# Optimization experiments

Hardware: AMD Instinct MI355X
Metric: run time of the kernel (lower is better)

## Reference

```python
import jax, jax.numpy as jnp
import numpy as np

N = 100_000      # nodes
E = 3_200_000    # edges (avg degree 32)
F_IN = 100       # raw feature dim (embedding Linear(100, 64))
H = 64           # in/hidden/out channels
C = 18           # class_num
EPS = 1e-12      # F.normalize eps


def _sage_conv(x, src, dst, edge_weight, Wl, bl, Wr):
    """PyG-style SAGEConv: mean-aggregate neighbor messages, two linears, L2 normalize."""
    msg = x[src]                                   # [E, d] gather of x_j
    if edge_weight is not None:
        msg = msg * edge_weight[:, None]
    agg = jax.ops.segment_sum(msg, dst, num_segments=N)                       # [N, d]
    deg = jax.ops.segment_sum(jnp.ones((src.shape[0],), x.dtype), dst, num_segments=N)
    mean = agg / jnp.maximum(deg, 1.0)[:, None]
    out = mean @ Wl + bl + x @ Wr                  # lin_l(aggr) + lin_r(root)
    nrm = jnp.sqrt(jnp.sum(out * out, axis=-1, keepdims=True))
    return out / jnp.maximum(nrm, EPS)


def setup_inputs() -> dict:
    key = jax.random.key(0)
    ks = jax.random.split(key, 16)
    s = 0.1
    inp = {
        "x": jax.random.normal(ks[0], (N, F_IN), jnp.float32),
        "edge_index": jax.random.randint(ks[1], (2, E), 0, N, dtype=jnp.int64),
        "edge_weight": jax.random.uniform(ks[2], (E,), jnp.float32),
        "emb_W": jax.random.normal(ks[3], (F_IN, H), jnp.float32) * s,
        "emb_b": jnp.zeros((H,), jnp.float32),
    }
    k = 4
    for i in (1, 2, 3):
        inp[f"Wl{i}"] = jax.random.normal(ks[k], (H, H), jnp.float32) * s; k += 1
        inp[f"bl{i}"] = jnp.zeros((H,), jnp.float32)
        inp[f"Wr{i}"] = jax.random.normal(ks[k], (H, H), jnp.float32) * s; k += 1
    inp["Wl4"] = jax.random.normal(ks[k], (H, C), jnp.float32) * s; k += 1
    inp["bl4"] = jnp.zeros((C,), jnp.float32)
    inp["Wr4"] = jax.random.normal(ks[k], (H, C), jnp.float32) * s
    return inp


def reference(x, edge_index, edge_weight, emb_W, emb_b,
              Wl1, bl1, Wr1, Wl2, bl2, Wr2, Wl3, bl3, Wr3,
              Wl4, bl4, Wr4):
    src, dst = edge_index[0], edge_index[1]
    h = jax.nn.relu(x @ emb_W + emb_b)             # embedding MLP
    for Wl, bl, Wr in ((Wl1, bl1, Wr1), (Wl2, bl2, Wr2), (Wl3, bl3, Wr3)):
        h = jax.nn.relu(_sage_conv(h, src, dst, edge_weight, Wl, bl, Wr))
        # dropout p=0.2 is identity in eval mode
    return _sage_conv(h, src, dst, None, Wl4, bl4, Wr4)
```

## Files before the change

kernel.cpp:

```cpp
#include <hip/hip_runtime.h>
#include <hip/hip_bf16.h>

#define N_NODES   100000
#define N_EDGES   3200000
#define F_IN      100
#define H_DIM     64
#define C_NUM     18
#define NPB       1024
#define N_BKT     98
#define EPB       8192

typedef __attribute__((ext_vector_type(8))) short short8;
typedef __attribute__((ext_vector_type(4))) float f32x4;

__device__ __forceinline__ float ldf(const void* p, long long i, int isbf) {
    if (isbf) return __bfloat162float(((const __hip_bfloat16*)p)[i]);
    return ((const float*)p)[i];
}
__device__ __forceinline__ int ldi(const void* p, long long i, int is64) {
    if (is64) return (int)(((const long long*)p)[i]);
    return ((const int*)p)[i];
}
__device__ __forceinline__ unsigned short f2us(float f) {
    __hip_bfloat16 b = __float2bfloat16(f);
    return *(unsigned short*)&b;
}

__global__ void detect_kernel(const void* ei, const void* x, int* flags)
{
    if (threadIdx.x != 0 || blockIdx.x != 0) return;
    const long long* e64 = (const long long*)ei;
    int ok64 = 1;
    for (int i = 0; i < 128; ++i) {
        long long v = e64[i];
        if (v < 0 || v >= N_NODES) { ok64 = 0; break; }
    }
    const __hip_bfloat16* xb = (const __hip_bfloat16*)x;
    int cnt = 0;
    for (int i = 0; i < 256; ++i) {
        float v = fabsf(__bfloat162float(xb[i]));
        if (v == 0.0f || (v > 9.5367431640625e-7f && v < 1.0e6f)) ++cnt;
    }
    flags[0] = ok64;
    flags[1] = (cnt >= 240) ? 1 : 0;
}

__global__ void zero98(int* __restrict__ pcnt)
{
    int i = threadIdx.x;
    if (i < N_BKT) pcnt[i] = 0;
}

__global__ __launch_bounds__(1024) void radix_count(const void* ei, int* __restrict__ pcnt,
                                                    const int* __restrict__ flags)
{
    __shared__ int hist[N_BKT];
    const int t = threadIdx.x;
    if (t < N_BKT) hist[t] = 0;
    __syncthreads();
    const int base = blockIdx.x * EPB;
    const int n = min(EPB, N_EDGES - base);
    const int is64 = flags[0];
    for (int j = t; j < n; j += 1024) {
        int d = ldi(ei, (long long)N_EDGES + base + j, is64);
        atomicAdd(&hist[d >> 10], 1);
    }
    __syncthreads();
    if (t < N_BKT) atomicAdd(&pcnt[t], hist[t]);
}

__global__ void scan98(const int* __restrict__ cnt, int* __restrict__ base,
                       int* __restrict__ cursor)
{
    __shared__ int tmp[128];
    const int t = threadIdx.x;
    int v = (t < N_BKT) ? cnt[t] : 0;
    tmp[t] = v;
    __syncthreads();
    for (int off = 1; off < 128; off <<= 1) {
        int add = (t >= off) ? tmp[t - off] : 0;
        __syncthreads();
        tmp[t] += add;
        __syncthreads();
    }
    if (t < N_BKT) { base[t] = tmp[t] - v; cursor[t] = tmp[t] - v; }
    if (t == 127) base[N_BKT] = tmp[127];
}

__global__ __launch_bounds__(1024) void radix_scatter(const void* ei, const void* ew,
                                                      int* __restrict__ gcursor,
                                                      uint2* __restrict__ temp,
                                                      const int* __restrict__ flags)
{
    __shared__ uint2 stage[EPB];
    __shared__ unsigned char stgb[EPB];
    __shared__ int hist[128], scan_s[128];
    __shared__ int gbase[N_BKT], lcur[N_BKT];
    const int t = threadIdx.x;
    if (t < 128) hist[t] = 0;
    __syncthreads();

    const int base = blockIdx.x * EPB;
    const int n = min(EPB, N_EDGES - base);
    const int is64 = flags[0], isbf = flags[1];

    int  bkt[8];
    uint2 pk[8];
#pragma unroll
    for (int j = 0; j < 8; ++j) {
        int i = j * 1024 + t;
        bkt[j] = -1;
        if (i < n) {
            int e = base + i;
            int s = ldi(ei, e, is64);
            int d = ldi(ei, (long long)N_EDGES + e, is64);
            float w = ldf(ew, e, isbf);
            bkt[j] = d >> 10;
            pk[j].x = (unsigned)s | ((unsigned)(d & (NPB - 1)) << 17);
            pk[j].y = (unsigned)f2us(w);
            atomicAdd(&hist[bkt[j]], 1);
        }
    }
    __syncthreads();
    if (t < 128) scan_s[t] = hist[t];
    __syncthreads();
    for (int off = 1; off < 128; off <<= 1) {
        int add = 0;
        if (t < 128 && t >= off) add = scan_s[t - off];
        __syncthreads();
        if (t < 128) scan_s[t] += add;
        __syncthreads();
    }
    if (t < N_BKT) {
        int excl = scan_s[t] - hist[t];
        lcur[t] = excl;
        gbase[t] = atomicAdd(&gcursor[t], hist[t]) - excl;
    }
    __syncthreads();
#pragma unroll
    for (int j = 0; j < 8; ++j) {
        if (bkt[j] >= 0) {
            int pos = atomicAdd(&lcur[bkt[j]], 1);
            stage[pos] = pk[j];
            stgb[pos] = (unsigned char)bkt[j];
        }
    }
    __syncthreads();
#pragma unroll
    for (int j = 0; j < 8; ++j) {
        int i = j * 1024 + t;
        if (i < n) {
            int b = stgb[i];
            temp[gbase[b] + i] = stage[i];
        }
    }
}

__global__ __launch_bounds__(1024) void csr_build(const uint2* __restrict__ temp,
                          const int* __restrict__ pbase,
                          unsigned int* __restrict__ csr_pk,
                          int* __restrict__ deg, int* __restrict__ row_start,
                          float* __restrict__ inv_deg)
{
    __shared__ int cnt[NPB], scan_s[NPB], cur[NPB];
    const int b = blockIdx.x;
    const int t = threadIdx.x;
    cnt[t] = 0;
    __syncthreads();
    const int bs = pbase[b];
    const int be = pbase[b + 1];
    for (int i = bs + t; i < be; i += NPB)
        atomicAdd(&cnt[(temp[i].x >> 17) & (NPB - 1)], 1);
    __syncthreads();
    int v = cnt[t];
    scan_s[t] = v;
    __syncthreads();
    for (int off = 1; off < NPB; off <<= 1) {
        int add = (t >= off) ? scan_s[t - off] : 0;
        __syncthreads();
        scan_s[t] += add;
        __syncthreads();
    }
    int excl = bs + scan_s[t] - v;
    cur[t] = excl;
    int node = b * NPB + t;
    if (node < N_NODES) {
        deg[node]       = v;
        row_start[node] = excl;
        inv_deg[node]   = 1.0f / (float)max(v, 1);
    }
    __syncthreads();
    for (int i = bs + t; i < be; i += NPB) {
        uint2 e = temp[i];
        int k = (e.x >> 17) & (NPB - 1);
        int pos = atomicAdd(&cur[k], 1);
        csr_pk[pos] = (e.x & 0x1FFFFu) | ((e.y & 0x7FFFu) << 17);
    }
}

__global__ void embed_mfma(const void* x, const void* W, const void* b,
                           __hip_bfloat16* __restrict__ h, const int* __restrict__ flags)
{
    constexpr int KP = 136;
    __shared__ unsigned short W_s[H_DIM * KP];
    __shared__ float b_s[H_DIM];
    const int t = threadIdx.x;
    const int isbf = flags[1];
    for (int i = t; i < 128 * H_DIM; i += 256) {
        int k = i >> 6, n = i & 63;
        float v = (k < F_IN) ? ldf(W, (long long)k * H_DIM + n, isbf) : 0.0f;
        W_s[n * KP + k] = f2us(v);
    }
    if (t < H_DIM) b_s[t] = ldf(b, t, isbf);
    __syncthreads();

    const int wave = t >> 6, lane = t & 63, c = lane & 15, quad = lane >> 4;
    short8 bfrag[4][4];
#pragma unroll
    for (int nt = 0; nt < 4; ++nt)
#pragma unroll
        for (int kt = 0; kt < 4; ++kt)
            bfrag[nt][kt] = *(const short8*)&W_s[(nt * 16 + c) * KP + kt * 32 + quad * 8];

    const int nb = (blockIdx.x * 4 + wave) * 16;
    if (nb >= N_NODES) return;
    int node = nb + c; if (node >= N_NODES) node = N_NODES - 1;

    short8 afrag[4];
#pragma unroll
    for (int kt = 0; kt < 4; ++kt) {
        short8 a;
#pragma unroll
        for (int j = 0; j < 8; ++j) {
            int k = kt * 32 + quad * 8 + j;
            float v = (k < F_IN) ? ldf(x, (long long)node * F_IN + k, isbf) : 0.0f;
            a[j] = (short)f2us(v);
        }
        afrag[kt] = a;
    }

    f32x4 acc[4] = {};
#pragma unroll
    for (int nt = 0; nt < 4; ++nt)
#pragma unroll
        for (int kt = 0; kt < 4; ++kt)
            acc[nt] = __builtin_amdgcn_mfma_f32_16x16x32_bf16(afrag[kt], bfrag[nt][kt], acc[nt], 0, 0, 0);

#pragma unroll
    for (int nt = 0; nt < 4; ++nt)
#pragma unroll
        for (int reg = 0; reg < 4; ++reg) {
            int nn = nb + quad * 4 + reg;
            int col = nt * 16 + c;
            if (nn < N_NODES) {
                float v = fmaxf(acc[nt][reg] + b_s[col], 0.0f);
                h[(size_t)nn * H_DIM + col] = __float2bfloat16(v);
            }
        }
}

template <bool USE_W>
__global__ void gather_mean(const __hip_bfloat16* __restrict__ h,
                            const unsigned int* __restrict__ csr_pk,
                            const int* __restrict__ row_start,
                            const int* __restrict__ deg,
                            const float* __restrict__ inv_deg,
                            __hip_bfloat16* __restrict__ mean)
{
    const int lane = threadIdx.x & 63;
    const int c = lane & 7;
    const int r = lane >> 3;
    const int wid = blockIdx.x * 4 + (threadIdx.x >> 6);
    const int nw  = gridDim.x * 4;

    for (int n = wid; n < N_NODES; n += nw) {
        const int start = row_start[n];
        const int d     = deg[n];
        unsigned int ev = 0;
        if (lane < d) ev = csr_pk[start + lane];
        const int dmain = min(d, 64);
        float a0 = 0.f, a1 = 0.f, a2 = 0.f, a3 = 0.f;
        float a4 = 0.f, a5 = 0.f, a6 = 0.f, a7 = 0.f;
#pragma unroll 2
        for (int j0 = 0; j0 < dmain; j0 += 8) {
            unsigned int e = __shfl(ev, j0 + r);
            int s = e & 0x1FFFF;
            float w;
            if (USE_W) w = __uint_as_float((e & 0xFFFE0000u) >> 1);
            else       w = (j0 + r < dmain) ? 1.0f : 0.0f;
            uint4 hv = *(const uint4*)(h + (size_t)s * H_DIM + 8 * c);
            a0 = fmaf(w, __uint_as_float(hv.x << 16),          a0);
            a1 = fmaf(w, __uint_as_float(hv.x & 0xFFFF0000u),  a1);
            a2 = fmaf(w, __uint_as_float(hv.y << 16),          a2);
            a3 = fmaf(w, __uint_as_float(hv.y & 0xFFFF0000u),  a3);
            a4 = fmaf(w, __uint_as_float(hv.z << 16),          a4);
            a5 = fmaf(w, __uint_as_float(hv.z & 0xFFFF0000u),  a5);
            a6 = fmaf(w, __uint_as_float(hv.w << 16),          a6);
            a7 = fmaf(w, __uint_as_float(hv.w & 0xFFFF0000u),  a7);
        }
        for (int j = 64 + r; j < d; j += 8) {
            unsigned int e = csr_pk[start + j];
            int s = e & 0x1FFFF;
            float w = USE_W ? __uint_as_float((e & 0xFFFE0000u) >> 1) : 1.0f;
            uint4 hv = *(const uint4*)(h + (size_t)s * H_DIM + 8 * c);
            a0 = fmaf(w, __uint_as_float(hv.x << 16),          a0);
            a1 = fmaf(w, __uint_as_float(hv.x & 0xFFFF0000u),  a1);
            a2 = fmaf(w, __uint_as_float(hv.y << 16),          a2);
            a3 = fmaf(w, __uint_as_float(hv.y & 0xFFFF0000u),  a3);
            a4 = fmaf(w, __uint_as_float(hv.z << 16),          a4);
            a5 = fmaf(w, __uint_as_float(hv.z & 0xFFFF0000u),  a5);
            a6 = fmaf(w, __uint_as_float(hv.w << 16),          a6);
            a7 = fmaf(w, __uint_as_float(hv.w & 0xFFFF0000u),  a7);
        }
#pragma unroll
        for (int m = 8; m <= 32; m <<= 1) {
            a0 += __shfl_xor(a0, m); a1 += __shfl_xor(a1, m);
            a2 += __shfl_xor(a2, m); a3 += __shfl_xor(a3, m);
            a4 += __shfl_xor(a4, m); a5 += __shfl_xor(a5, m);
            a6 += __shfl_xor(a6, m); a7 += __shfl_xor(a7, m);
        }
        if (r == 0) {
            float inv = inv_deg[n];
            uint4 st;
            st.x = (unsigned)f2us(a0 * inv) | ((unsigned)f2us(a1 * inv) << 16);
            st.y = (unsigned)f2us(a2 * inv) | ((unsigned)f2us(a3 * inv) << 16);
            st.z = (unsigned)f2us(a4 * inv) | ((unsigned)f2us(a5 * inv) << 16);
            st.w = (unsigned)f2us(a6 * inv) | ((unsigned)f2us(a7 * inv) << 16);
            *(uint4*)(mean + (size_t)n * H_DIM + 8 * c) = st;
        }
    }
}

template <int COUT, bool RELU, bool FINAL>
__global__ void transform_mfma(const __hip_bfloat16* __restrict__ meanp,
                               const __hip_bfloat16* __restrict__ hp,
                               const void* Wl, const void* bl, const void* Wr,
                               __hip_bfloat16* __restrict__ h_out,
                               const int* __restrict__ flags, void* dout)
{
    constexpr int CP = (COUT + 15) & ~15;
    constexpr int NT = CP / 16;
    constexpr int KP = 136;
    __shared__ unsigned short W_s[CP * KP];
    __shared__ float b_s[CP];
    const int t = threadIdx.x;
    const int isbf = flags[1];
    for (int i = t; i < 128 * CP; i += 256) {
        int k = i / CP, n = i % CP;
        float v = 0.0f;
        if (n < COUT)
            v = (k < 64) ? ldf(Wl, (long long)k * COUT + n, isbf)
                         : ldf(Wr, (long long)(k - 64) * COUT + n, isbf);
        W_s[n * KP + k] = f2us(v);
    }
    if (t < CP) b_s[t] = (t < COUT) ? ldf(bl, t, isbf) : 0.0f;
    __syncthreads();

    const int wave = t >> 6, lane = t & 63, c = lane & 15, quad = lane >> 4;
    short8 bfrag[NT][4];
#pragma unroll
    for (int nt = 0; nt < NT; ++nt)
#pragma unroll
        for (int kt = 0; kt < 4; ++kt)
            bfrag[nt][kt] = *(const short8*)&W_s[(nt * 16 + c) * KP + kt * 32 + quad * 8];

    const int nb = (blockIdx.x * 4 + wave) * 16;
    if (nb >= N_NODES) return;
    int node = nb + c; if (node >= N_NODES) node = N_NODES - 1;

    short8 afrag[4];
#pragma unroll
    for (int kt = 0; kt < 4; ++kt) {
        const __hip_bfloat16* sp = (kt < 2) ? meanp : hp;
        afrag[kt] = *(const short8*)(sp + (size_t)node * H_DIM + (kt & 1) * 32 + quad * 8);
    }

    f32x4 acc[NT] = {};
#pragma unroll
    for (int nt = 0; nt < NT; ++nt)
#pragma unroll
        for (int kt = 0; kt < 4; ++kt)
            acc[nt] = __builtin_amdgcn_mfma_f32_16x16x32_bf16(afrag[kt], bfrag[nt][kt], acc[nt], 0, 0, 0);

    float rs[4];
#pragma unroll
    for (int reg = 0; reg < 4; ++reg) {
        float s2 = 0.f;
#pragma unroll
        for (int nt = 0; nt < NT; ++nt) {
            float v = acc[nt][reg] + b_s[nt * 16 + c];
            acc[nt][reg] = v;
            s2 += v * v;
        }
        s2 += __shfl_xor(s2, 1); s2 += __shfl_xor(s2, 2);
        s2 += __shfl_xor(s2, 4); s2 += __shfl_xor(s2, 8);
        rs[reg] = 1.0f / fmaxf(sqrtf(s2), 1e-12f);
    }

#pragma unroll
    for (int nt = 0; nt < NT; ++nt)
#pragma unroll
        for (int reg = 0; reg < 4; ++reg) {
            int nn  = nb + quad * 4 + reg;
            int col = nt * 16 + c;
            if (nn < N_NODES && col < COUT) {
                float v = acc[nt][reg] * rs[reg];
                if (RELU) v = fmaxf(v, 0.0f);
                if (FINAL) {
                    if (isbf) ((__hip_bfloat16*)dout)[(size_t)nn * COUT + col] = __float2bfloat16(v);
                    else      ((float*)dout)[(size_t)nn * COUT + col] = v;
                } else {
                    h_out[(size_t)nn * H_DIM + col] = __float2bfloat16(v);
                }
            }
        }
}

extern "C" void kernel_launch(void* const* d_in, const int* in_sizes, int n_in,
                              void* d_out, int out_size, void* d_ws, size_t ws_size,
                              hipStream_t stream)
{
    const void* x    = d_in[0];
    const void* ei   = d_in[1];
    const void* ew   = d_in[2];
    const void* embW = d_in[3];
    const void* embB = d_in[4];
    const void* Wl1 = d_in[5];  const void* bl1 = d_in[6];  const void* Wr1 = d_in[7];
    const void* Wl2 = d_in[8];  const void* bl2 = d_in[9];  const void* Wr2 = d_in[10];
    const void* Wl3 = d_in[11]; const void* bl3 = d_in[12]; const void* Wr3 = d_in[13];
    const void* Wl4 = d_in[14]; const void* bl4 = d_in[15]; const void* Wr4 = d_in[16];
    (void)in_sizes; (void)n_in; (void)out_size; (void)ws_size;

    char* ws = (char*)d_ws;
    size_t off = 0;
    auto alloc = [&](size_t bytes) -> void* {
        void* p = ws + off;
        off += (bytes + 255) & ~(size_t)255;
        return p;
    };
    uint2* temp = (uint2*)alloc((size_t)N_EDGES * sizeof(uint2));
    __hip_bfloat16* hA = (__hip_bfloat16*)temp;
    __hip_bfloat16* hB = (__hip_bfloat16*)((char*)temp + (size_t)N_NODES * H_DIM * 2);
    unsigned int* csr_pk = (unsigned int*)alloc((size_t)N_EDGES * sizeof(unsigned int));
    int*   pcnt    = (int*)  alloc((N_BKT)     * sizeof(int));
    int*   pbase   = (int*)  alloc((N_BKT + 1) * sizeof(int));
    int*   pcursor = (int*)  alloc((N_BKT)     * sizeof(int));
    int*   deg     = (int*)  alloc((size_t)N_NODES * sizeof(int));
    int*   row_st  = (int*)  alloc((size_t)N_NODES * sizeof(int));
    float* inv_deg = (float*)alloc((size_t)N_NODES * sizeof(float));
    int*   flags   = (int*)  alloc(256);

    const int NBr = (N_EDGES + EPB - 1) / EPB;
    const int NBt = (N_NODES + 63) / 64;

    detect_kernel<<<1, 64, 0, stream>>>(ei, x, flags);
    zero98<<<1, 128, 0, stream>>>(pcnt);
    radix_count<<<NBr, 1024, 0, stream>>>(ei, pcnt, flags);
    scan98<<<1, 128, 0, stream>>>(pcnt, pbase, pcursor);
    radix_scatter<<<NBr, 1024, 0, stream>>>(ei, ew, pcursor, temp, flags);
    csr_build<<<N_BKT, NPB, 0, stream>>>(temp, pbase, csr_pk, deg, row_st, inv_deg);

    embed_mfma<<<NBt, 256, 0, stream>>>(x, embW, embB, hA, flags);

    gather_mean<true><<<2048, 256, 0, stream>>>(hA, csr_pk, row_st, deg, inv_deg, hB);
    transform_mfma<H_DIM, true, false><<<NBt, 256, 0, stream>>>(
        hB, hA, Wl1, bl1, Wr1, hB, flags, d_out);
    gather_mean<true><<<2048, 256, 0, stream>>>(hB, csr_pk, row_st, deg, inv_deg, hA);
    transform_mfma<H_DIM, true, false><<<NBt, 256, 0, stream>>>(
        hA, hB, Wl2, bl2, Wr2, hA, flags, d_out);
    gather_mean<true><<<2048, 256, 0, stream>>>(hA, csr_pk, row_st, deg, inv_deg, hB);
    transform_mfma<H_DIM, true, false><<<NBt, 256, 0, stream>>>(
        hB, hA, Wl3, bl3, Wr3, hB, flags, d_out);
    gather_mean<false><<<2048, 256, 0, stream>>>(hB, csr_pk, row_st, deg, inv_deg, hA);
    transform_mfma<C_NUM, false, true><<<NBt, 256, 0, stream>>>(
        hA, hB, Wl4, bl4, Wr4, nullptr, flags, d_out);
}
```

Measured before the change: 551.4 us.

## Fuse neighbor mean aggregation with SAGE transform via shared-memory mean tile

Merges the gather_mean and transform_mfma kernels into one sage_fused kernel. Each block aggregates 64 nodes into a shared-memory mean tile, then runs the MFMA transform and normalization directly from it, which removes the global round trip of the mean tensor and four kernel launches. The embedding kernel now stages the x tile in shared memory with coalesced loads, and weight staging writes vectorized short8 rows. The gather now uses a fixed grid of 1563 blocks with 16 nodes per wave done sequentially, replacing the 2048-block grid-stride loop. This may reduce latency hiding and occupancy for the irregular gather, and the larger shared-memory footprint per block adds further occupancy pressure.

```diff
diff --git a/kernel.cpp b/kernel.cpp
--- a/kernel.cpp
+++ b/kernel.cpp
@@ -203,15 +203,50 @@
 {
     constexpr int KP = 136;
     __shared__ unsigned short W_s[H_DIM * KP];
+    __shared__ unsigned short x_s[64 * KP];
     __shared__ float b_s[H_DIM];
     const int t = threadIdx.x;
     const int isbf = flags[1];
-    for (int i = t; i < 128 * H_DIM; i += 256) {
-        int k = i >> 6, n = i & 63;
-        float v = (k < F_IN) ? ldf(W, (long long)k * H_DIM + n, isbf) : 0.0f;
-        W_s[n * KP + k] = f2us(v);
+
+    {
+        const int n0 = t >> 4, k8 = t & 15;
+        for (int n = n0; n < H_DIM; n += 16) {
+            union { unsigned short u[8]; short8 v; } tmp;
+#pragma unroll
+            for (int j = 0; j < 8; ++j) {
+                int k = k8 * 8 + j;
+                tmp.u[j] = (k < F_IN) ? f2us(ldf(W, (long long)k * H_DIM + n, isbf))
+                                      : (unsigned short)0;
+            }
+            *(short8*)&W_s[n * KP + k8 * 8] = tmp.v;
+        }
     }
     if (t < H_DIM) b_s[t] = ldf(b, t, isbf);
+
+    const int nb0 = blockIdx.x * 64;
+    const int valid = min(64, N_NODES - nb0);
+    if (isbf) {
+        const uint2* xu = (const uint2*)x + (size_t)nb0 * 25;
+        for (int i2 = t; i2 < valid * 25; i2 += 256) {
+            int row = i2 / 25, col4 = i2 - row * 25;
+            *(uint2*)&x_s[row * KP + col4 * 4] = xu[i2];
+        }
+    } else {
+        for (int i = t; i < valid * 100; i += 256) {
+            int row = i / 100, col = i - row * 100;
+            x_s[row * KP + col] = f2us(((const float*)x)[(size_t)(nb0 + row) * 100 + col]);
+        }
+    }
+    for (int i = t; i < 64 * 32; i += 256) {
+        int row = i >> 5, col = 100 + (i & 31);
+        x_s[row * KP + col] = 0;
+    }
+    if (valid < 64) {
+        for (int i = t; i < (64 - valid) * 100; i += 256) {
+            int row = valid + i / 100, col = i % 100;
+            x_s[row * KP + col] = 0;
+        }
+    }
     __syncthreads();
 
     const int wave = t >> 6, lane = t & 63, c = lane & 15, quad = lane >> 4;
@@ -222,22 +257,10 @@
         for (int kt = 0; kt < 4; ++kt)
             bfrag[nt][kt] = *(const short8*)&W_s[(nt * 16 + c) * KP + kt * 32 + quad * 8];
 
-    const int nb = (blockIdx.x * 4 + wave) * 16;
-    if (nb >= N_NODES) return;
-    int node = nb + c; if (node >= N_NODES) node = N_NODES - 1;
-
     short8 afrag[4];
 #pragma unroll
-    for (int kt = 0; kt < 4; ++kt) {
-        short8 a;
-#pragma unroll
-        for (int j = 0; j < 8; ++j) {
-            int k = kt * 32 + quad * 8 + j;
-            float v = (k < F_IN) ? ldf(x, (long long)node * F_IN + k, isbf) : 0.0f;
-            a[j] = (short)f2us(v);
-        }
-        afrag[kt] = a;
-    }
+    for (int kt = 0; kt < 4; ++kt)
+        afrag[kt] = *(const short8*)&x_s[(wave * 16 + c) * KP + kt * 32 + quad * 8];
 
     f32x4 acc[4] = {};
 #pragma unroll
@@ -246,6 +269,7 @@
         for (int kt = 0; kt < 4; ++kt)
             acc[nt] = __builtin_amdgcn_mfma_f32_16x16x32_bf16(afrag[kt], bfrag[nt][kt], acc[nt], 0, 0, 0);
 
+    const int nb = nb0 + wave * 16;
 #pragma unroll
     for (int nt = 0; nt < 4; ++nt)
 #pragma unroll
@@ -259,21 +283,56 @@
         }
 }
 
-template <bool USE_W>
-__global__ void gather_mean(const __hip_bfloat16* __restrict__ h,
-                            const unsigned int* __restrict__ csr_pk,
-                            const int* __restrict__ row_start,
-                            const int* __restrict__ deg,
-                            const float* __restrict__ inv_deg,
-                            __hip_bfloat16* __restrict__ mean)
-{
-    const int lane = threadIdx.x & 63;
-    const int c = lane & 7;
-    const int r = lane >> 3;
-    const int wid = blockIdx.x * 4 + (threadIdx.x >> 6);
-    const int nw  = gridDim.x * 4;
-
-    for (int n = wid; n < N_NODES; n += nw) {
+template <int COUT, bool RELU, bool USE_W, bool FINAL>
+__global__ void sage_fused(const __hip_bfloat16* __restrict__ h_in,
+                           const unsigned int* __restrict__ csr_pk,
+                           const int* __restrict__ row_start,
+                           const int* __restrict__ deg,
+                           const float* __restrict__ inv_deg,
+                           const void* Wl, const void* bl, const void* Wr,
+                           __hip_bfloat16* __restrict__ h_out,
+                           const int* __restrict__ flags, void* dout)
+{
+    constexpr int CP = (COUT + 15) & ~15;
+    constexpr int NT = CP / 16;
+    constexpr int KP = 136;
+    constexpr int MP = 72;
+    __shared__ unsigned short W_s[CP * KP];
+    __shared__ unsigned short mean_s[64 * MP];
+    __shared__ float b_s[CP];
+    const int t = threadIdx.x;
+    const int isbf = flags[1];
+
+    {
+        const int n0 = t >> 4, k8 = t & 15;
+        for (int n = n0; n < CP; n += 16) {
+            union { unsigned short u[8]; short8 v; } tmp;
+#pragma unroll
+            for (int j = 0; j < 8; ++j) {
+                int k = k8 * 8 + j;
+                float v = 0.0f;
+                if (n < COUT)
+                    v = (k < 64) ? ldf(Wl, (long long)k * COUT + n, isbf)
+                                 : ldf(Wr, (long long)(k - 64) * COUT + n, isbf);
+                tmp.u[j] = f2us(v);
+            }
+            *(short8*)&W_s[n * KP + k8 * 8] = tmp.v;
+        }
+    }
+    if (t < CP) b_s[t] = (t < COUT) ? ldf(bl, t, isbf) : 0.0f;
+
+    const int wave = t >> 6, lane = t & 63;
+    const int c8 = lane & 7;
+    const int r  = lane >> 3;
+    const int nb = blockIdx.x * 64;
+
+    for (int i = 0; i < 16; ++i) {
+        const int row = wave * 16 + i;
+        const int n = nb + row;
+        if (n >= N_NODES) {
+            if (r == 0) { short8 z = {}; *(short8*)&mean_s[row * MP + c8 * 8] = z; }
+            continue;
+        }
         const int start = row_start[n];
         const int d     = deg[n];
         unsigned int ev = 0;
@@ -288,7 +347,7 @@
             float w;
             if (USE_W) w = __uint_as_float((e & 0xFFFE0000u) >> 1);
             else       w = (j0 + r < dmain) ? 1.0f : 0.0f;
-            uint4 hv = *(const uint4*)(h + (size_t)s * H_DIM + 8 * c);
+            uint4 hv = *(const uint4*)(h_in + (size_t)s * H_DIM + 8 * c8);
             a0 = fmaf(w, __uint_as_float(hv.x << 16),          a0);
             a1 = fmaf(w, __uint_as_float(hv.x & 0xFFFF0000u),  a1);
             a2 = fmaf(w, __uint_as_float(hv.y << 16),          a2);
@@ -302,7 +361,7 @@
             unsigned int e = csr_pk[start + j];
             int s = e & 0x1FFFF;
             float w = USE_W ? __uint_as_float((e & 0xFFFE0000u) >> 1) : 1.0f;
-            uint4 hv = *(const uint4*)(h + (size_t)s * H_DIM + 8 * c);
+            uint4 hv = *(const uint4*)(h_in + (size_t)s * H_DIM + 8 * c8);
             a0 = fmaf(w, __uint_as_float(hv.x << 16),          a0);
             a1 = fmaf(w, __uint_as_float(hv.x & 0xFFFF0000u),  a1);
             a2 = fmaf(w, __uint_as_float(hv.y << 16),          a2);
@@ -321,42 +380,17 @@
         }
         if (r == 0) {
             float inv = inv_deg[n];
-            uint4 st;
-            st.x = (unsigned)f2us(a0 * inv) | ((unsigned)f2us(a1 * inv) << 16);
-            st.y = (unsigned)f2us(a2 * inv) | ((unsigned)f2us(a3 * inv) << 16);
-            st.z = (unsigned)f2us(a4 * inv) | ((unsigned)f2us(a5 * inv) << 16);
-            st.w = (unsigned)f2us(a6 * inv) | ((unsigned)f2us(a7 * inv) << 16);
-            *(uint4*)(mean + (size_t)n * H_DIM + 8 * c) = st;
-        }
-    }
-}
-
-template <int COUT, bool RELU, bool FINAL>
-__global__ void transform_mfma(const __hip_bfloat16* __restrict__ meanp,
-                               const __hip_bfloat16* __restrict__ hp,
-                               const void* Wl, const void* bl, const void* Wr,
-                               __hip_bfloat16* __restrict__ h_out,
-                               const int* __restrict__ flags, void* dout)
-{
-    constexpr int CP = (COUT + 15) & ~15;
-    constexpr int NT = CP / 16;
-    constexpr int KP = 136;
-    __shared__ unsigned short W_s[CP * KP];
-    __shared__ float b_s[CP];
-    const int t = threadIdx.x;
-    const int isbf = flags[1];
-    for (int i = t; i < 128 * CP; i += 256) {
-        int k = i / CP, n = i % CP;
-        float v = 0.0f;
-        if (n < COUT)
-            v = (k < 64) ? ldf(Wl, (long long)k * COUT + n, isbf)
-                         : ldf(Wr, (long long)(k - 64) * COUT + n, isbf);
-        W_s[n * KP + k] = f2us(v);
-    }
-    if (t < CP) b_s[t] = (t < COUT) ? ldf(bl, t, isbf) : 0.0f;
-    __syncthreads();
-
-    const int wave = t >> 6, lane = t & 63, c = lane & 15, quad = lane >> 4;
+            union { unsigned short u[8]; short8 v; } st;
+            st.u[0] = f2us(a0 * inv); st.u[1] = f2us(a1 * inv);
+            st.u[2] = f2us(a2 * inv); st.u[3] = f2us(a3 * inv);
+            st.u[4] = f2us(a4 * inv); st.u[5] = f2us(a5 * inv);
+            st.u[6] = f2us(a6 * inv); st.u[7] = f2us(a7 * inv);
+            *(short8*)&mean_s[row * MP + c8 * 8] = st.v;
+        }
+    }
+    __syncthreads();
+
+    const int c = lane & 15, quad = lane >> 4;
     short8 bfrag[NT][4];
 #pragma unroll
     for (int nt = 0; nt < NT; ++nt)
@@ -364,15 +398,16 @@
         for (int kt = 0; kt < 4; ++kt)
             bfrag[nt][kt] = *(const short8*)&W_s[(nt * 16 + c) * KP + kt * 32 + quad * 8];
 
-    const int nb = (blockIdx.x * 4 + wave) * 16;
-    if (nb >= N_NODES) return;
-    int node = nb + c; if (node >= N_NODES) node = N_NODES - 1;
+    const int nbw = nb + wave * 16;
+    int node = nbw + c; if (node >= N_NODES) node = N_NODES - 1;
 
     short8 afrag[4];
 #pragma unroll
     for (int kt = 0; kt < 4; ++kt) {
-        const __hip_bfloat16* sp = (kt < 2) ? meanp : hp;
-        afrag[kt] = *(const short8*)(sp + (size_t)node * H_DIM + (kt & 1) * 32 + quad * 8);
+        if (kt < 2)
+            afrag[kt] = *(const short8*)&mean_s[(wave * 16 + c) * MP + kt * 32 + quad * 8];
+        else
+            afrag[kt] = *(const short8*)(h_in + (size_t)node * H_DIM + (kt - 2) * 32 + quad * 8);
     }
 
     f32x4 acc[NT] = {};
@@ -401,7 +436,7 @@
     for (int nt = 0; nt < NT; ++nt)
 #pragma unroll
         for (int reg = 0; reg < 4; ++reg) {
-            int nn  = nb + quad * 4 + reg;
+            int nn  = nbw + quad * 4 + reg;
             int col = nt * 16 + c;
             if (nn < N_NODES && col < COUT) {
                 float v = acc[nt][reg] * rs[reg];
@@ -462,16 +497,12 @@
 
     embed_mfma<<<NBt, 256, 0, stream>>>(x, embW, embB, hA, flags);
 
-    gather_mean<true><<<2048, 256, 0, stream>>>(hA, csr_pk, row_st, deg, inv_deg, hB);
-    transform_mfma<H_DIM, true, false><<<NBt, 256, 0, stream>>>(
-        hB, hA, Wl1, bl1, Wr1, hB, flags, d_out);
-    gather_mean<true><<<2048, 256, 0, stream>>>(hB, csr_pk, row_st, deg, inv_deg, hA);
-    transform_mfma<H_DIM, true, false><<<NBt, 256, 0, stream>>>(
-        hA, hB, Wl2, bl2, Wr2, hA, flags, d_out);
-    gather_mean<true><<<2048, 256, 0, stream>>>(hA, csr_pk, row_st, deg, inv_deg, hB);
-    transform_mfma<H_DIM, true, false><<<NBt, 256, 0, stream>>>(
-        hB, hA, Wl3, bl3, Wr3, hB, flags, d_out);
-    gather_mean<false><<<2048, 256, 0, stream>>>(hB, csr_pk, row_st, deg, inv_deg, hA);
-    transform_mfma<C_NUM, false, true><<<NBt, 256, 0, stream>>>(
-        hA, hB, Wl4, bl4, Wr4, nullptr, flags, d_out);
-}
+    sage_fused<H_DIM, true,  true,  false><<<NBt, 256, 0, stream>>>(
+        hA, csr_pk, row_st, deg, inv_deg, Wl1, bl1, Wr1, hB, flags, d_out);
+    sage_fused<H_DIM, true,  true,  false><<<NBt, 256, 0, stream>>>(
+        hB, csr_pk, row_st, deg, inv_deg, Wl2, bl2, Wr2, hA, flags, d_out);
+    sage_fused<H_DIM, true,  true,  false><<<NBt, 256, 0, stream>>>(
+        hA, csr_pk, row_st, deg, inv_deg, Wl3, bl3, Wr3, hB, flags, d_out);
+    sage_fused<C_NUM, false, false, true ><<<NBt, 256, 0, stream>>>(
+        hB, csr_pk, row_st, deg, inv_deg, Wl4, bl4, Wr4, nullptr, flags, d_out);
+}
```

Result: slower. 694.9 us (+26.0%).
